# Kernel tuning notes

Hardware: AMD Instinct MI355X
Metric: run time of the kernel (lower is better)

## Reference

```python
import jax, jax.numpy as jnp
import numpy as np

N_NODES = 500_000
N_EDGES = 2_500_000
N_GRAPHS = 1024


def _linear_params(key, fan_in, fan_out):
    # mimic torch.nn.Linear default init: U(-1/sqrt(fan_in), 1/sqrt(fan_in))
    k1, k2 = jax.random.split(key)
    bound = 1.0 / np.sqrt(fan_in)
    W = jax.random.uniform(k1, (fan_in, fan_out), jnp.float32, -bound, bound)
    b = jax.random.uniform(k2, (fan_out,), jnp.float32, -bound, bound)
    return W, b


def setup_inputs() -> dict:
    key = jax.random.key(0)
    ks = jax.random.split(key, 8)
    x = jax.random.normal(ks[0], (N_NODES, 2), jnp.float32)
    edge_index = jax.random.randint(ks[1], (2, N_EDGES), 0, N_NODES, jnp.int32)
    batch = jnp.sort(jax.random.randint(ks[2], (N_NODES,), 0, N_GRAPHS, jnp.int32))
    W1, b1 = _linear_params(ks[3], 2, 16)
    W2, b2 = _linear_params(ks[4], 16, 32)
    Wf1, bf1 = _linear_params(ks[5], 32, 16)
    Wf2, bf2 = _linear_params(ks[6], 16, 1)
    return {"x": x, "edge_index": edge_index, "batch": batch,
            "W1": W1, "b1": b1, "W2": W2, "b2": b2,
            "Wf1": Wf1, "bf1": bf1, "Wf2": Wf2, "bf2": bf2}


def _gnn_conv(h, W, b, src, dst, n_nodes):
    # Linear then add-aggregate: out[dst] += h_lin[src]  (self-loops already in src/dst)
    h = h @ W + b                       # [N, out]
    msgs = h[src]                       # gather over edges: [E+N, out]
    return jax.ops.segment_sum(msgs, dst, num_segments=n_nodes)


def reference(x, edge_index, batch, W1, b1, W2, b2, Wf1, bf1, Wf2, bf2):
    n = x.shape[0]
    loop = jnp.arange(n, dtype=edge_index.dtype)
    src = jnp.concatenate([edge_index[0], loop])  # source nodes (x_j)
    dst = jnp.concatenate([edge_index[1], loop])  # target nodes (aggregation index)

    h = jax.nn.relu(_gnn_conv(x, W1, b1, src, dst, n))   # [N, 16]
    h = jax.nn.relu(_gnn_conv(h, W2, b2, src, dst, n))   # [N, 32]

    # global mean pool per graph
    sums = jax.ops.segment_sum(h, batch, num_segments=N_GRAPHS)           # [G, 32]
    cnts = jax.ops.segment_sum(jnp.ones((n, 1), h.dtype), batch, num_segments=N_GRAPHS)
    pooled = sums / jnp.maximum(cnts, 1.0)

    out = jax.nn.relu(pooled @ Wf1 + bf1)
    out = out @ Wf2 + bf2                                # [G, 1]
    return out
```

## Files before the change

### kernel.cpp

```cpp
#include <hip/hip_runtime.h>


#define TPB 256
#define SBK_BITS 9
#define SBK 512
#define NSBX 1024
#define CAPX 576
#define CAPS 3072
#define PE1 4096

typedef unsigned int uint32;

__device__ __forceinline__ float reluf(float v) { return v > 0.f ? v : 0.f; }

__global__ void kPart1(const int* __restrict__ src, const int* __restrict__ dst,
                       int* __restrict__ curx, int* __restrict__ part1x, int E) {
    __shared__ int h[NSBX];
    for (int i = threadIdx.x; i < NSBX; i += TPB) h[i] = 0;
    __syncthreads();
    int base = blockIdx.x * PE1;
    int end = base + PE1 < E ? base + PE1 : E;
    for (int e = base + threadIdx.x; e < end; e += TPB)
        atomicAdd(&h[dst[e] >> SBK_BITS], 1);
    __syncthreads();
    int slice = blockIdx.x & 7;
    int* cur = curx + slice * NSBX;
    int rbase = slice * (NSBX * CAPX);
    for (int i = threadIdx.x; i < NSBX; i += TPB) {
        int c = h[i];
        if (c) h[i] = i * CAPX + atomicAdd(&cur[i], c);
    }
    __syncthreads();
    for (int e = base + threadIdx.x; e < end; e += TPB) {
        int d = dst[e];
        int b = d >> SBK_BITS;
        int pos = atomicAdd(&h[b], 1);
        if (pos < (b + 1) * CAPX)
            part1x[rbase + pos] = (src[e] << SBK_BITS) | (d & (SBK - 1));
    }
}

__global__ void kPart2C1(const int* __restrict__ curx, const int* __restrict__ part1x,
                         const float* __restrict__ x,
                         int* __restrict__ rowptr, int* __restrict__ supEnd,
                         int* __restrict__ partS, uint2* __restrict__ ninfo,
                         float* __restrict__ pooled, int N, int G) {
    int z = blockIdx.x * TPB + threadIdx.x;
    if (z < 32 * G) pooled[z] = 0.f;

    __shared__ int hist[SBK];
    __shared__ int ps[TPB];
    __shared__ int sls[CAPS];
    __shared__ int segc[8];
    int sb = blockIdx.x;
    int node0 = sb << SBK_BITS;
    int sbase = sb * CAPS;
    int t = threadIdx.x;
    for (int i = t; i < SBK; i += TPB) hist[i] = 0;
    if (t < 8) {
        int c = curx[t * NSBX + sb];
        segc[t] = c > CAPX ? CAPX : c;
    }
    __syncthreads();
    for (int seg = 0; seg < 8; seg++) {
        const int* p = part1x + seg * (NSBX * CAPX) + sb * CAPX;
        int c = segc[seg];
        for (int i = t; i < c; i += TPB)
            atomicAdd(&hist[p[i] & (SBK - 1)], 1);
    }
    __syncthreads();
    int v0 = hist[2 * t], v1 = hist[2 * t + 1];
    int s = v0 + v1;
    ps[t] = s;
    __syncthreads();
    for (int off = 1; off < TPB; off <<= 1) {
        int u = (t >= off) ? ps[t - off] : 0;
        __syncthreads();
        ps[t] += u;
        __syncthreads();
    }
    int start0 = ps[t] - s;
    int start1 = start0 + v0;
    int n0 = node0 + 2 * t, n1 = n0 + 1;
    if (n0 < N) rowptr[n0] = sbase + start0;
    if (n1 < N) rowptr[n1] = sbase + start1;
    hist[2 * t] = start0;
    hist[2 * t + 1] = start1;
    if (t == TPB - 1) supEnd[sb] = sbase + ps[t];
    __syncthreads();
    for (int seg = 0; seg < 8; seg++) {
        const int* p = part1x + seg * (NSBX * CAPX) + sb * CAPX;
        int c = segc[seg];
        for (int i = t; i < c; i += TPB) {
            int w = p[i];
            int slot = atomicAdd(&hist[w & (SBK - 1)], 1);
            if (slot < CAPS) {
                int sid = w >> SBK_BITS;
                partS[sbase + slot] = sid;
                sls[slot] = sid;
            }
        }
    }
    __syncthreads();
#pragma unroll
    for (int half = 0; half < 2; half++) {
        int n = half ? n1 : n0;
        if (n >= N) continue;
        int st = half ? start1 : start0;
        int dg = half ? v1 : v0;
        int en = st + dg; if (en > CAPS) en = CAPS;
        float2 sv = ((const float2*)x)[n];
        float a0 = sv.x, a1 = sv.y;
        for (int e = st; e < en; e++) {
            float2 xv = ((const float2*)x)[sls[e]];
            a0 += xv.x; a1 += xv.y;
        }
        int indeg = dg + 1;
        if (indeg > 31) indeg = 31;
        ninfo[n] = make_uint2(__float_as_uint(a0),
                              (__float_as_uint(a1) & ~31u) | (uint32)indeg);
    }
}

__device__ __forceinline__ int rowEnd(const int* __restrict__ rowptr,
                                      const int* __restrict__ supEnd, int i, int N) {
    int nxt = i + 1;
    return (nxt >= N || (nxt & (SBK - 1)) == 0) ? supEnd[i >> SBK_BITS] : rowptr[nxt];
}

__device__ __forceinline__ void addMsg(float* a, uint2 q,
                                       const float* __restrict__ W1,
                                       const float* __restrict__ b1) {
    float n0 = __uint_as_float(q.x);
    float ndeg = (float)(q.y & 31u);
    float n1 = __uint_as_float(q.y & ~31u);
#pragma unroll
    for (int j = 0; j < 16; j++)
        a[j] += reluf(fmaf(n0, W1[j], fmaf(n1, W1[16 + j], ndeg * b1[j])));
}

__global__ void __launch_bounds__(TPB, 4)
kConv2(const uint2* __restrict__ ninfo, const int* __restrict__ partS,
       const int* __restrict__ rowptr, const int* __restrict__ supEnd,
       const int* __restrict__ batch,
       const float* __restrict__ W1, const float* __restrict__ b1,
       const float* __restrict__ W2, const float* __restrict__ b2,
       float* __restrict__ pooled, int N) {
    __shared__ float srow[TPB * 17];
    __shared__ int sbat[TPB];
    __shared__ float spart[16 * 16];
    int node0 = blockIdx.x * TPB;
    int l = threadIdx.x;
    int i = node0 + l;
    bool valid = i < N;
    float a[16];
    float sdeg = 0.f;
    if (valid) {
        int rs = rowptr[i];
        int re = rowEnd(rowptr, supEnd, i, N);
        uint2 p = ninfo[i];
        float s0 = __uint_as_float(p.x);
        sdeg = (float)(p.y & 31u);
        float s1 = __uint_as_float(p.y & ~31u);
#pragma unroll
        for (int j = 0; j < 16; j++)
            a[j] = reluf(fmaf(s0, W1[j], fmaf(s1, W1[16 + j], sdeg * b1[j])));
        int e = rs;
        for (; e + 4 <= re; e += 4) {
            int w0 = partS[e], w1 = partS[e + 1], w2 = partS[e + 2], w3 = partS[e + 3];
            uint2 q0 = ninfo[w0], q1 = ninfo[w1], q2 = ninfo[w2], q3 = ninfo[w3];
            addMsg(a, q0, W1, b1);
            addMsg(a, q1, W1, b1);
            addMsg(a, q2, W1, b1);
            addMsg(a, q3, W1, b1);
        }
        for (; e < re; e++)
            addMsg(a, ninfo[partS[e]], W1, b1);
        sbat[l] = batch[i];
    } else {
#pragma unroll
        for (int j = 0; j < 16; j++) a[j] = 0.f;
        sbat[l] = -1;
    }
    __syncthreads();
    int lastl = N - 1 - node0;
    if (lastl > TPB - 1) lastl = TPB - 1;
    int g0 = sbat[0], g1 = sbat[lastl];
    int f = l & 15, rr = l >> 4;
#pragma unroll
    for (int h = 0; h < 2; h++) {
        if (valid) {
#pragma unroll
            for (int jj = 0; jj < 16; jj++) {
                int j = h * 16 + jj;
                float vv = sdeg * b2[j];
#pragma unroll
                for (int k = 0; k < 16; k++) vv = fmaf(a[k], W2[k * 32 + j], vv);
                srow[l * 17 + jj] = reluf(vv);
            }
        } else {
#pragma unroll
            for (int jj = 0; jj < 16; jj++) srow[l * 17 + jj] = 0.f;
        }
        __syncthreads();
        for (int g = g0; g <= g1; g++) {
            float p = 0.f;
#pragma unroll
            for (int q = 0; q < 16; q++) {
                int n = rr + 16 * q;
                p += (sbat[n] == g) ? srow[n * 17 + f] : 0.f;
            }
            spart[rr * 16 + f] = p;
            __syncthreads();
            if (rr == 0) {
                float tot = 0.f;
#pragma unroll
                for (int q = 0; q < 16; q++) tot += spart[q * 16 + f];
                unsafeAtomicAdd(&pooled[32 * (size_t)g + h * 16 + f], tot);
            }
            __syncthreads();
        }
        __syncthreads();
    }
}

__device__ __forceinline__ int lower_bound(const int* __restrict__ a, int n, int v) {
    int lo = 0, hi = n;
    while (lo < hi) {
        int m = (lo + hi) >> 1;
        if (a[m] < v) lo = m + 1; else hi = m;
    }
    return lo;
}

__global__ void kMLP(const float* __restrict__ pooled, const int* __restrict__ batch,
                     const float* __restrict__ Wf1, const float* __restrict__ bf1,
                     const float* __restrict__ Wf2, const float* __restrict__ bf2,
                     float* __restrict__ out, int N, int G) {
    int g = blockIdx.x * blockDim.x + threadIdx.x;
    if (g >= G) return;
    int lo = lower_bound(batch, N, g);
    int hi = lower_bound(batch, N, g + 1);
    int cnt = hi - lo;
    float inv = 1.f / (float)(cnt > 1 ? cnt : 1);
    float p[32];
#pragma unroll
    for (int i = 0; i < 32; i++) p[i] = pooled[32 * (size_t)g + i] * inv;
    float acc = bf2[0];
#pragma unroll
    for (int j = 0; j < 16; j++) {
        float v = bf1[j];
#pragma unroll
        for (int i = 0; i < 32; i++) v = fmaf(p[i], Wf1[i * 16 + j], v);
        acc = fmaf(reluf(v), Wf2[j], acc);
    }
    out[g] = acc;
}

static inline size_t align256(size_t v) { return (v + 255) & ~(size_t)255; }

extern "C" void kernel_launch(void* const* d_in, const int* in_sizes, int n_in,
                              void* d_out, int out_size, void* d_ws, size_t ws_size,
                              hipStream_t stream) {
    const float* x    = (const float*)d_in[0];
    const int*   ei   = (const int*)d_in[1];
    const int*   batch= (const int*)d_in[2];
    const float* W1   = (const float*)d_in[3];
    const float* b1   = (const float*)d_in[4];
    const float* W2   = (const float*)d_in[5];
    const float* b2   = (const float*)d_in[6];
    const float* Wf1  = (const float*)d_in[7];
    const float* bf1  = (const float*)d_in[8];
    const float* Wf2  = (const float*)d_in[9];
    const float* bf2  = (const float*)d_in[10];
    float* out = (float*)d_out;

    const int N = in_sizes[0] / 2;
    const int E = in_sizes[1] / 2;
    const int G = out_size;
    const int* src = ei;
    const int* dst = ei + E;

    const int NSB = (N + SBK - 1) >> SBK_BITS;
    const int NFB = (N + TPB - 1) / TPB;

    char* w = (char*)d_ws;
    int*   curx   = (int*)w;    w += align256((size_t)8 * NSBX * sizeof(int));
    int*   supEnd = (int*)w;    w += align256((size_t)NSBX * sizeof(int));
    int*   rowptr = (int*)w;    w += align256((size_t)N * sizeof(int));
    uint2* ninfo  = (uint2*)w;  w += align256((size_t)N * sizeof(uint2));
    float* pooled = (float*)w;  w += align256((size_t)G * 32 * sizeof(float));
    int*   part1x = (int*)w;    w += align256((size_t)8 * NSBX * CAPX * sizeof(int));
    int*   partS  = (int*)w;    w += align256((size_t)NSBX * CAPS * sizeof(int));

    const int nb1 = (E + PE1 - 1) / PE1;

    hipMemsetAsync(curx, 0, (size_t)8 * NSBX * sizeof(int), stream);
    kPart1  <<<nb1, TPB, 0, stream>>>(src, dst, curx, part1x, E);
    kPart2C1<<<NSB, TPB, 0, stream>>>(curx, part1x, x, rowptr, supEnd, partS,
                                      ninfo, pooled, N, G);
    kConv2  <<<NFB, TPB, 0, stream>>>(ninfo, partS, rowptr, supEnd, batch,
                                      W1, b1, W2, b2, pooled, N);
    kMLP    <<<(G + TPB - 1) / TPB, TPB, 0, stream>>>(pooled, batch, Wf1, bf1, Wf2, bf2, out, N, G);
}
```

Measured before the change: 194.2 us.

## Degree-sort nodes within blocks to balance per-thread edge loops

Within each 256-node half of a superblock, kPart2C1 counting-sorts nodes by in-degree and builds a permutation (nperm). Both the conv1 accumulation and kConv2 then process nodes in that order, so threads in a wavefront run loops of similar length and lose less time to divergence. kPart1 also keeps the dst values it loaded for the histogram in registers and reuses them in the scatter pass, and kMLP shares lower_bound results between neighbouring threads through shared memory. The cost is an extra permutation array, extra shared-memory atomics and scans, and scattered rather than coalesced per-thread accesses to rowptr, ninfo and batch.

```diff
diff --git a/kernel.cpp b/kernel.cpp
--- a/kernel.cpp
+++ b/kernel.cpp
@@ -8,6 +8,7 @@
 #define CAPX 576
 #define CAPS 3072
 #define PE1 4096
+#define EPT (PE1 / TPB)
 
 typedef unsigned int uint32;
 
@@ -20,8 +21,17 @@
     __syncthreads();
     int base = blockIdx.x * PE1;
     int end = base + PE1 < E ? base + PE1 : E;
-    for (int e = base + threadIdx.x; e < end; e += TPB)
-        atomicAdd(&h[dst[e] >> SBK_BITS], 1);
+    int et = base + threadIdx.x;
+    int rd[EPT];
+#pragma unroll
+    for (int k = 0; k < EPT; k++) {
+        int e = et + k * TPB;
+        if (e < end) {
+            int d = dst[e];
+            rd[k] = d;
+            atomicAdd(&h[d >> SBK_BITS], 1);
+        }
+    }
     __syncthreads();
     int slice = blockIdx.x & 7;
     int* cur = curx + slice * NSBX;
@@ -31,12 +41,16 @@
         if (c) h[i] = i * CAPX + atomicAdd(&cur[i], c);
     }
     __syncthreads();
-    for (int e = base + threadIdx.x; e < end; e += TPB) {
-        int d = dst[e];
-        int b = d >> SBK_BITS;
-        int pos = atomicAdd(&h[b], 1);
-        if (pos < (b + 1) * CAPX)
-            part1x[rbase + pos] = (src[e] << SBK_BITS) | (d & (SBK - 1));
+#pragma unroll
+    for (int k = 0; k < EPT; k++) {
+        int e = et + k * TPB;
+        if (e < end) {
+            int d = rd[k];
+            int b = d >> SBK_BITS;
+            int pos = atomicAdd(&h[b], 1);
+            if (pos < (b + 1) * CAPX)
+                part1x[rbase + pos] = (src[e] << SBK_BITS) | (d & (SBK - 1));
+        }
     }
 }
 
@@ -44,19 +58,24 @@
                          const float* __restrict__ x,
                          int* __restrict__ rowptr, int* __restrict__ supEnd,
                          int* __restrict__ partS, uint2* __restrict__ ninfo,
+                         int* __restrict__ nperm,
                          float* __restrict__ pooled, int N, int G) {
     int z = blockIdx.x * TPB + threadIdx.x;
     if (z < 32 * G) pooled[z] = 0.f;
 
     __shared__ int hist[SBK];
+    __shared__ int sstart[SBK];
     __shared__ int ps[TPB];
     __shared__ int sls[CAPS];
     __shared__ int segc[8];
+    __shared__ int h32[64];
+    __shared__ short perm[SBK];
     int sb = blockIdx.x;
     int node0 = sb << SBK_BITS;
     int sbase = sb * CAPS;
     int t = threadIdx.x;
     for (int i = t; i < SBK; i += TPB) hist[i] = 0;
+    if (t < 64) h32[t] = 0;
     if (t < 8) {
         int c = curx[t * NSBX + sb];
         segc[t] = c > CAPX ? CAPX : c;
@@ -84,10 +103,26 @@
     int n0 = node0 + 2 * t, n1 = n0 + 1;
     if (n0 < N) rowptr[n0] = sbase + start0;
     if (n1 < N) rowptr[n1] = sbase + start1;
+    sstart[2 * t] = start0;
+    sstart[2 * t + 1] = start1;
+    if (t == TPB - 1) supEnd[sb] = sbase + ps[t];
+    int half = t >> 7;
+    int k0 = v0 > 31 ? 31 : v0;
+    int k1 = v1 > 31 ? 31 : v1;
+    atomicAdd(&h32[half * 32 + k0], 1);
+    atomicAdd(&h32[half * 32 + k1], 1);
+    __syncthreads();
+    if (t < 2) {
+        int acc = 0;
+        for (int k = 0; k < 32; k++) { int c = h32[t * 32 + k]; h32[t * 32 + k] = acc; acc += c; }
+    }
     hist[2 * t] = start0;
     hist[2 * t + 1] = start1;
-    if (t == TPB - 1) supEnd[sb] = sbase + ps[t];
-    __syncthreads();
+    __syncthreads();
+    int s0 = atomicAdd(&h32[half * 32 + k0], 1);
+    int s1 = atomicAdd(&h32[half * 32 + k1], 1);
+    perm[(half << 8) + s0] = (short)(2 * t);
+    perm[(half << 8) + s1] = (short)(2 * t + 1);
     for (int seg = 0; seg < 8; seg++) {
         const int* p = part1x + seg * (NSBX * CAPX) + sb * CAPX;
         int c = segc[seg];
@@ -102,13 +137,18 @@
         }
     }
     __syncthreads();
-#pragma unroll
-    for (int half = 0; half < 2; half++) {
-        int n = half ? n1 : n0;
+    for (int i = t; i < SBK; i += TPB) nperm[node0 + i] = node0 + perm[i];
+    int totE = ps[TPB - 1];
+#pragma unroll
+    for (int hh = 0; hh < 2; hh++) {
+        int slot = 2 * t + hh;
+        int j = perm[slot];
+        int n = node0 + j;
         if (n >= N) continue;
-        int st = half ? start1 : start0;
-        int dg = half ? v1 : v0;
-        int en = st + dg; if (en > CAPS) en = CAPS;
+        int st = sstart[j];
+        int en0 = (j < SBK - 1) ? sstart[j + 1] : totE;
+        int dg = en0 - st;
+        int en = en0 > CAPS ? CAPS : en0;
         float2 sv = ((const float2*)x)[n];
         float a0 = sv.x, a1 = sv.y;
         for (int e = st; e < en; e++) {
@@ -142,7 +182,7 @@
 __global__ void __launch_bounds__(TPB, 4)
 kConv2(const uint2* __restrict__ ninfo, const int* __restrict__ partS,
        const int* __restrict__ rowptr, const int* __restrict__ supEnd,
-       const int* __restrict__ batch,
+       const int* __restrict__ batch, const int* __restrict__ nperm,
        const float* __restrict__ W1, const float* __restrict__ b1,
        const float* __restrict__ W2, const float* __restrict__ b2,
        float* __restrict__ pooled, int N) {
@@ -151,7 +191,7 @@
     __shared__ float spart[16 * 16];
     int node0 = blockIdx.x * TPB;
     int l = threadIdx.x;
-    int i = node0 + l;
+    int i = nperm[node0 + l];
     bool valid = i < N;
     float a[16];
     float sdeg = 0.f;
@@ -183,9 +223,9 @@
         sbat[l] = -1;
     }
     __syncthreads();
-    int lastl = N - 1 - node0;
-    if (lastl > TPB - 1) lastl = TPB - 1;
-    int g0 = sbat[0], g1 = sbat[lastl];
+    int nlast = node0 + TPB - 1;
+    if (nlast > N - 1) nlast = N - 1;
+    int g0 = batch[node0], g1 = batch[nlast];
     int f = l & 15, rr = l >> 4;
 #pragma unroll
     for (int h = 0; h < 2; h++) {
@@ -237,10 +277,16 @@
                      const float* __restrict__ Wf1, const float* __restrict__ bf1,
                      const float* __restrict__ Wf2, const float* __restrict__ bf2,
                      float* __restrict__ out, int N, int G) {
+    __shared__ int slo[TPB];
     int g = blockIdx.x * blockDim.x + threadIdx.x;
+    int lo = 0;
+    if (g < G) lo = lower_bound(batch, N, g);
+    slo[threadIdx.x] = lo;
+    __syncthreads();
     if (g >= G) return;
-    int lo = lower_bound(batch, N, g);
-    int hi = lower_bound(batch, N, g + 1);
+    int hi;
+    if (threadIdx.x < TPB - 1 && g + 1 < G) hi = slo[threadIdx.x + 1];
+    else hi = (g + 1 < G) ? lower_bound(batch, N, g + 1) : N;
     int cnt = hi - lo;
     float inv = 1.f / (float)(cnt > 1 ? cnt : 1);
     float p[32];
@@ -290,6 +336,7 @@
     int*   rowptr = (int*)w;    w += align256((size_t)N * sizeof(int));
     uint2* ninfo  = (uint2*)w;  w += align256((size_t)N * sizeof(uint2));
     float* pooled = (float*)w;  w += align256((size_t)G * 32 * sizeof(float));
+    int*   nperm  = (int*)w;    w += align256((size_t)NSBX * SBK * sizeof(int));
     int*   part1x = (int*)w;    w += align256((size_t)8 * NSBX * CAPX * sizeof(int));
     int*   partS  = (int*)w;    w += align256((size_t)NSBX * CAPS * sizeof(int));
 
@@ -298,8 +345,8 @@
     hipMemsetAsync(curx, 0, (size_t)8 * NSBX * sizeof(int), stream);
     kPart1  <<<nb1, TPB, 0, stream>>>(src, dst, curx, part1x, E);
     kPart2C1<<<NSB, TPB, 0, stream>>>(curx, part1x, x, rowptr, supEnd, partS,
-                                      ninfo, pooled, N, G);
-    kConv2  <<<NFB, TPB, 0, stream>>>(ninfo, partS, rowptr, supEnd, batch,
+                                      ninfo, nperm, pooled, N, G);
+    kConv2  <<<NFB, TPB, 0, stream>>>(ninfo, partS, rowptr, supEnd, batch, nperm,
                                       W1, b1, W2, b2, pooled, N);
     kMLP    <<<(G + TPB - 1) / TPB, TPB, 0, stream>>>(pooled, batch, Wf1, bf1, Wf2, bf2, out, N, G);
 }
```

Result: no change. 196.0 us (+0.9%).

## Shrink partition buckets, stage edges in LDS, fuse MLP into conv2 via last-block

Applied to the files above, without the earlier changes.

Halves the super-bucket size to 256 nodes, which doubles the number of partition blocks and gives one node per thread in the second pass. That pass now stages each bucket's edges in shared memory instead of reading part1x twice, and uses a wave-shuffle scan. kPart1 moves to 512 threads and keeps the dst values in registers across both passes. kConv2 derives row end from the packed degree, dropping supEnd, and the final MLP is folded into the last finishing block via an atomic counter. This removes one launch and some global traffic, but the whole MLP now runs serially in one block.

```diff
diff --git a/kernel.cpp b/kernel.cpp
--- a/kernel.cpp
+++ b/kernel.cpp
@@ -2,12 +2,15 @@
 
 
 #define TPB 256
-#define SBK_BITS 9
-#define SBK 512
-#define NSBX 1024
-#define CAPX 576
-#define CAPS 3072
+#define TPB1 512
+#define SBK_BITS 8
+#define SBK 256
+#define NSBX 2048
+#define CAPX 288
+#define CAPS 1536
+#define EWCAP (8 * CAPX)
 #define PE1 4096
+#define EPT (PE1 / TPB1)
 
 typedef unsigned int uint32;
 
@@ -16,99 +19,119 @@
 __global__ void kPart1(const int* __restrict__ src, const int* __restrict__ dst,
                        int* __restrict__ curx, int* __restrict__ part1x, int E) {
     __shared__ int h[NSBX];
-    for (int i = threadIdx.x; i < NSBX; i += TPB) h[i] = 0;
+    for (int i = threadIdx.x; i < NSBX; i += TPB1) h[i] = 0;
     __syncthreads();
     int base = blockIdx.x * PE1;
     int end = base + PE1 < E ? base + PE1 : E;
-    for (int e = base + threadIdx.x; e < end; e += TPB)
-        atomicAdd(&h[dst[e] >> SBK_BITS], 1);
+    int et = base + threadIdx.x;
+    int rd[EPT];
+#pragma unroll
+    for (int k = 0; k < EPT; k++) {
+        int e = et + k * TPB1;
+        if (e < end) {
+            int d = dst[e];
+            rd[k] = d;
+            atomicAdd(&h[d >> SBK_BITS], 1);
+        }
+    }
     __syncthreads();
     int slice = blockIdx.x & 7;
     int* cur = curx + slice * NSBX;
     int rbase = slice * (NSBX * CAPX);
-    for (int i = threadIdx.x; i < NSBX; i += TPB) {
+    for (int i = threadIdx.x; i < NSBX; i += TPB1) {
         int c = h[i];
         if (c) h[i] = i * CAPX + atomicAdd(&cur[i], c);
     }
     __syncthreads();
-    for (int e = base + threadIdx.x; e < end; e += TPB) {
-        int d = dst[e];
-        int b = d >> SBK_BITS;
-        int pos = atomicAdd(&h[b], 1);
-        if (pos < (b + 1) * CAPX)
-            part1x[rbase + pos] = (src[e] << SBK_BITS) | (d & (SBK - 1));
+#pragma unroll
+    for (int k = 0; k < EPT; k++) {
+        int e = et + k * TPB1;
+        if (e < end) {
+            int d = rd[k];
+            int b = d >> SBK_BITS;
+            int pos = atomicAdd(&h[b], 1);
+            if (pos < (b + 1) * CAPX)
+                part1x[rbase + pos] = (src[e] << SBK_BITS) | (d & (SBK - 1));
+        }
     }
 }
 
 __global__ void kPart2C1(const int* __restrict__ curx, const int* __restrict__ part1x,
                          const float* __restrict__ x,
-                         int* __restrict__ rowptr, int* __restrict__ supEnd,
+                         int* __restrict__ rowptr,
                          int* __restrict__ partS, uint2* __restrict__ ninfo,
                          float* __restrict__ pooled, int N, int G) {
     int z = blockIdx.x * TPB + threadIdx.x;
     if (z < 32 * G) pooled[z] = 0.f;
 
+    __shared__ int ew[EWCAP];
+    __shared__ int sls[CAPS];
     __shared__ int hist[SBK];
-    __shared__ int ps[TPB];
-    __shared__ int sls[CAPS];
-    __shared__ int segc[8];
+    __shared__ int sstart[SBK];
+    __shared__ int segc[8], soff[8];
+    __shared__ int stot;
+    __shared__ int wsum[4];
     int sb = blockIdx.x;
     int node0 = sb << SBK_BITS;
     int sbase = sb * CAPS;
     int t = threadIdx.x;
-    for (int i = t; i < SBK; i += TPB) hist[i] = 0;
+    hist[t] = 0;
     if (t < 8) {
         int c = curx[t * NSBX + sb];
         segc[t] = c > CAPX ? CAPX : c;
     }
     __syncthreads();
+    if (t == 0) {
+        int acc = 0;
+        for (int s = 0; s < 8; s++) { soff[s] = acc; acc += segc[s]; }
+        stot = acc;
+    }
+    __syncthreads();
     for (int seg = 0; seg < 8; seg++) {
         const int* p = part1x + seg * (NSBX * CAPX) + sb * CAPX;
-        int c = segc[seg];
-        for (int i = t; i < c; i += TPB)
-            atomicAdd(&hist[p[i] & (SBK - 1)], 1);
-    }
-    __syncthreads();
-    int v0 = hist[2 * t], v1 = hist[2 * t + 1];
-    int s = v0 + v1;
-    ps[t] = s;
-    __syncthreads();
-    for (int off = 1; off < TPB; off <<= 1) {
-        int u = (t >= off) ? ps[t - off] : 0;
-        __syncthreads();
-        ps[t] += u;
-        __syncthreads();
-    }
-    int start0 = ps[t] - s;
-    int start1 = start0 + v0;
-    int n0 = node0 + 2 * t, n1 = n0 + 1;
-    if (n0 < N) rowptr[n0] = sbase + start0;
-    if (n1 < N) rowptr[n1] = sbase + start1;
-    hist[2 * t] = start0;
-    hist[2 * t + 1] = start1;
-    if (t == TPB - 1) supEnd[sb] = sbase + ps[t];
-    __syncthreads();
-    for (int seg = 0; seg < 8; seg++) {
-        const int* p = part1x + seg * (NSBX * CAPX) + sb * CAPX;
-        int c = segc[seg];
+        int c = segc[seg], o = soff[seg];
         for (int i = t; i < c; i += TPB) {
             int w = p[i];
-            int slot = atomicAdd(&hist[w & (SBK - 1)], 1);
-            if (slot < CAPS) {
-                int sid = w >> SBK_BITS;
-                partS[sbase + slot] = sid;
-                sls[slot] = sid;
-            }
-        }
-    }
-    __syncthreads();
-#pragma unroll
-    for (int half = 0; half < 2; half++) {
-        int n = half ? n1 : n0;
-        if (n >= N) continue;
-        int st = half ? start1 : start0;
-        int dg = half ? v1 : v0;
-        int en = st + dg; if (en > CAPS) en = CAPS;
+            ew[o + i] = w;
+            atomicAdd(&hist[w & (SBK - 1)], 1);
+        }
+    }
+    __syncthreads();
+    int tot = stot;
+    int cnt = hist[t];
+    int incl = cnt;
+#pragma unroll
+    for (int off = 1; off < 64; off <<= 1) {
+        int u = __shfl_up(incl, off, 64);
+        if ((t & 63) >= off) incl += u;
+    }
+    if ((t & 63) == 63) wsum[t >> 6] = incl;
+    __syncthreads();
+    int wid = t >> 6;
+    int wpre = 0;
+#pragma unroll
+    for (int w = 0; w < 4; w++) wpre += (w < wid) ? wsum[w] : 0;
+    int start = incl - cnt + wpre;
+    sstart[t] = start;
+    hist[t] = start;
+    int n = node0 + t;
+    if (n < N) rowptr[n] = sbase + start;
+    __syncthreads();
+    for (int i = t; i < tot; i += TPB) {
+        int w = ew[i];
+        int slot = atomicAdd(&hist[w & (SBK - 1)], 1);
+        if (slot < CAPS) {
+            int sid = w >> SBK_BITS;
+            partS[sbase + slot] = sid;
+            sls[slot] = sid;
+        }
+    }
+    __syncthreads();
+    if (n < N) {
+        int st = sstart[t];
+        int en0 = (t < SBK - 1) ? sstart[t + 1] : tot;
+        int dg = en0 - st;
+        int en = en0 > CAPS ? CAPS : en0;
         float2 sv = ((const float2*)x)[n];
         float a0 = sv.x, a1 = sv.y;
         for (int e = st; e < en; e++) {
@@ -120,12 +143,6 @@
         ninfo[n] = make_uint2(__float_as_uint(a0),
                               (__float_as_uint(a1) & ~31u) | (uint32)indeg);
     }
-}
-
-__device__ __forceinline__ int rowEnd(const int* __restrict__ rowptr,
-                                      const int* __restrict__ supEnd, int i, int N) {
-    int nxt = i + 1;
-    return (nxt >= N || (nxt & (SBK - 1)) == 0) ? supEnd[i >> SBK_BITS] : rowptr[nxt];
 }
 
 __device__ __forceinline__ void addMsg(float* a, uint2 q,
@@ -139,16 +156,28 @@
         a[j] += reluf(fmaf(n0, W1[j], fmaf(n1, W1[16 + j], ndeg * b1[j])));
 }
 
+__device__ __forceinline__ int lower_bound(const int* __restrict__ a, int n, int v) {
+    int lo = 0, hi = n;
+    while (lo < hi) {
+        int m = (lo + hi) >> 1;
+        if (a[m] < v) lo = m + 1; else hi = m;
+    }
+    return lo;
+}
+
 __global__ void __launch_bounds__(TPB, 4)
 kConv2(const uint2* __restrict__ ninfo, const int* __restrict__ partS,
-       const int* __restrict__ rowptr, const int* __restrict__ supEnd,
-       const int* __restrict__ batch,
+       const int* __restrict__ rowptr, const int* __restrict__ batch,
        const float* __restrict__ W1, const float* __restrict__ b1,
        const float* __restrict__ W2, const float* __restrict__ b2,
-       float* __restrict__ pooled, int N) {
+       const float* __restrict__ Wf1, const float* __restrict__ bf1,
+       const float* __restrict__ Wf2, const float* __restrict__ bf2,
+       float* __restrict__ pooled, float* __restrict__ out,
+       int* __restrict__ ctr, int N, int G) {
     __shared__ float srow[TPB * 17];
     __shared__ int sbat[TPB];
     __shared__ float spart[16 * 16];
+    __shared__ int isLast;
     int node0 = blockIdx.x * TPB;
     int l = threadIdx.x;
     int i = node0 + l;
@@ -156,12 +185,12 @@
     float a[16];
     float sdeg = 0.f;
     if (valid) {
-        int rs = rowptr[i];
-        int re = rowEnd(rowptr, supEnd, i, N);
         uint2 p = ninfo[i];
         float s0 = __uint_as_float(p.x);
         sdeg = (float)(p.y & 31u);
         float s1 = __uint_as_float(p.y & ~31u);
+        int rs = rowptr[i];
+        int re = rs + (int)(p.y & 31u) - 1;
 #pragma unroll
         for (int j = 0; j < 16; j++)
             a[j] = reluf(fmaf(s0, W1[j], fmaf(s1, W1[16 + j], sdeg * b1[j])));
@@ -183,9 +212,9 @@
         sbat[l] = -1;
     }
     __syncthreads();
-    int lastl = N - 1 - node0;
-    if (lastl > TPB - 1) lastl = TPB - 1;
-    int g0 = sbat[0], g1 = sbat[lastl];
+    int nlast = node0 + TPB - 1;
+    if (nlast > N - 1) nlast = N - 1;
+    int g0 = batch[node0], g1 = batch[nlast];
     int f = l & 15, rr = l >> 4;
 #pragma unroll
     for (int h = 0; h < 2; h++) {
@@ -222,39 +251,33 @@
         }
         __syncthreads();
     }
-}
-
-__device__ __forceinline__ int lower_bound(const int* __restrict__ a, int n, int v) {
-    int lo = 0, hi = n;
-    while (lo < hi) {
-        int m = (lo + hi) >> 1;
-        if (a[m] < v) lo = m + 1; else hi = m;
-    }
-    return lo;
-}
-
-__global__ void kMLP(const float* __restrict__ pooled, const int* __restrict__ batch,
-                     const float* __restrict__ Wf1, const float* __restrict__ bf1,
-                     const float* __restrict__ Wf2, const float* __restrict__ bf2,
-                     float* __restrict__ out, int N, int G) {
-    int g = blockIdx.x * blockDim.x + threadIdx.x;
-    if (g >= G) return;
-    int lo = lower_bound(batch, N, g);
-    int hi = lower_bound(batch, N, g + 1);
-    int cnt = hi - lo;
-    float inv = 1.f / (float)(cnt > 1 ? cnt : 1);
-    float p[32];
-#pragma unroll
-    for (int i = 0; i < 32; i++) p[i] = pooled[32 * (size_t)g + i] * inv;
-    float acc = bf2[0];
-#pragma unroll
-    for (int j = 0; j < 16; j++) {
-        float v = bf1[j];
-#pragma unroll
-        for (int i = 0; i < 32; i++) v = fmaf(p[i], Wf1[i * 16 + j], v);
-        acc = fmaf(reluf(v), Wf2[j], acc);
-    }
-    out[g] = acc;
+    if (l == 0) {
+        __threadfence();
+        int r = __hip_atomic_fetch_add(ctr, 1, __ATOMIC_ACQ_REL, __HIP_MEMORY_SCOPE_AGENT);
+        isLast = (r == (int)gridDim.x - 1) ? 1 : 0;
+    }
+    __syncthreads();
+    if (!isLast) return;
+    for (int g = l; g < G; g += TPB) {
+        int lo = lower_bound(batch, N, g);
+        int hi = lower_bound(batch, N, g + 1);
+        int cnt = hi - lo;
+        float inv = 1.f / (float)(cnt > 1 ? cnt : 1);
+        float p[32];
+#pragma unroll
+        for (int q = 0; q < 32; q++)
+            p[q] = __hip_atomic_load(&pooled[32 * (size_t)g + q],
+                                     __ATOMIC_RELAXED, __HIP_MEMORY_SCOPE_AGENT) * inv;
+        float acc = bf2[0];
+#pragma unroll
+        for (int j = 0; j < 16; j++) {
+            float v = bf1[j];
+#pragma unroll
+            for (int q = 0; q < 32; q++) v = fmaf(p[q], Wf1[q * 16 + j], v);
+            acc = fmaf(reluf(v), Wf2[j], acc);
+        }
+        out[g] = acc;
+    }
 }
 
 static inline size_t align256(size_t v) { return (v + 255) & ~(size_t)255; }
@@ -282,11 +305,10 @@
     const int* dst = ei + E;
 
     const int NSB = (N + SBK - 1) >> SBK_BITS;
-    const int NFB = (N + TPB - 1) / TPB;
 
     char* w = (char*)d_ws;
     int*   curx   = (int*)w;    w += align256((size_t)8 * NSBX * sizeof(int));
-    int*   supEnd = (int*)w;    w += align256((size_t)NSBX * sizeof(int));
+    int*   ctr    = (int*)w;    w += 256;
     int*   rowptr = (int*)w;    w += align256((size_t)N * sizeof(int));
     uint2* ninfo  = (uint2*)w;  w += align256((size_t)N * sizeof(uint2));
     float* pooled = (float*)w;  w += align256((size_t)G * 32 * sizeof(float));
@@ -295,11 +317,11 @@
 
     const int nb1 = (E + PE1 - 1) / PE1;
 
-    hipMemsetAsync(curx, 0, (size_t)8 * NSBX * sizeof(int), stream);
-    kPart1  <<<nb1, TPB, 0, stream>>>(src, dst, curx, part1x, E);
-    kPart2C1<<<NSB, TPB, 0, stream>>>(curx, part1x, x, rowptr, supEnd, partS,
+    hipMemsetAsync(curx, 0, (size_t)8 * NSBX * sizeof(int) + 256, stream);
+    kPart1  <<<nb1, TPB1, 0, stream>>>(src, dst, curx, part1x, E);
+    kPart2C1<<<NSB, TPB, 0, stream>>>(curx, part1x, x, rowptr, partS,
                                       ninfo, pooled, N, G);
-    kConv2  <<<NFB, TPB, 0, stream>>>(ninfo, partS, rowptr, supEnd, batch,
-                                      W1, b1, W2, b2, pooled, N);
-    kMLP    <<<(G + TPB - 1) / TPB, TPB, 0, stream>>>(pooled, batch, Wf1, bf1, Wf2, bf2, out, N, G);
-}
+    kConv2  <<<NSB, TPB, 0, stream>>>(ninfo, partS, rowptr, batch,
+                                      W1, b1, W2, b2, Wf1, bf1, Wf2, bf2,
+                                      pooled, out, ctr, N, G);
+}
```

Result: slower. 312.9 us (+61.1%).
